# Optimization experiments

Measured on AMD Instinct MI355X. Metric: run time of the kernel, lower is better.

Reference implementation:

```python
import jax, jax.numpy as jnp
import numpy as np

N = 8192          # tokens
CD = 512          # coarse_dim
FD = 512          # fine_dim
CB = 4096         # coarse codebook size
FB = 8192         # fine codebook size
COST = 0.25       # commitment cost
LRELU = 0.1
EPS = 1e-5


def _vq(x, emb):
    # squared-distance cdist: [n, K]
    d = jnp.sum(x * x, axis=1, keepdims=True) + jnp.sum(emb * emb, axis=1) - 2.0 * (x @ emb.T)
    idx = jnp.argmin(d, axis=1)          # temperature=1.0 (updates=0); scaling doesn't change argmin
    q = emb[idx]                          # gather == one-hot @ emb, without materializing one-hot
    e_loss = jnp.mean((jax.lax.stop_gradient(q) - x) ** 2)
    q_loss = jnp.mean((q - jax.lax.stop_gradient(x)) ** 2)
    loss = q_loss + COST * e_loss
    q_st = x + jax.lax.stop_gradient(q - x)   # straight-through
    return q_st, loss


def _mlp(x, w, b, g, be):
    # Linear (torch: x @ W.T + b) -> LayerNorm -> LeakyReLU(0.1)
    h = x @ w.T + b
    m = jnp.mean(h, axis=-1, keepdims=True)
    v = jnp.var(h, axis=-1, keepdims=True)
    h = (h - m) / jnp.sqrt(v + EPS) * g + be
    return jnp.where(h > 0, h, LRELU * h)


def setup_inputs() -> dict:
    key = jax.random.key(0)
    ks = jax.random.split(key, 6)
    xav_c = float(np.sqrt(6.0 / (CB + CD)))
    xav_f = float(np.sqrt(6.0 / (FB + FD)))
    lin_s = float(np.sqrt(1.0 / CD))
    return {
        'z': jax.random.normal(ks[0], (N, CD + FD), dtype=jnp.float32),
        'coarse_emb': jax.random.uniform(ks[1], (CB, CD), jnp.float32, -xav_c, xav_c),
        'fine_emb': jax.random.uniform(ks[2], (FB, FD), jnp.float32, -xav_f, xav_f),
        'w_c2f': jax.random.uniform(ks[3], (FD, CD), jnp.float32, -lin_s, lin_s),
        'b_c2f': jnp.zeros((FD,), jnp.float32),
        'g_c2f': jnp.ones((FD,), jnp.float32),
        'be_c2f': jnp.zeros((FD,), jnp.float32),
        'w_f2c': jax.random.uniform(ks[4], (CD, FD), jnp.float32, -lin_s, lin_s),
        'b_f2c': jnp.zeros((CD,), jnp.float32),
        'g_f2c': jnp.ones((CD,), jnp.float32),
        'be_f2c': jnp.zeros((CD,), jnp.float32),
        'gate_c_raw': jnp.float32(0.5),
        'gate_f_raw': jnp.float32(0.5),
    }


def reference(z, coarse_emb, fine_emb, w_c2f, b_c2f, g_c2f, be_c2f,
              w_f2c, b_f2c, g_f2c, be_f2c, gate_c_raw, gate_f_raw):
    split = z.shape[1] // 2
    z_coarse, z_fine = z[:, :split], z[:, split:]

    z_coarse_q, coarse_loss = _vq(z_coarse, coarse_emb)
    coarse_influence = _mlp(jax.lax.stop_gradient(z_coarse_q), w_c2f, b_c2f, g_c2f, be_c2f)
    gate_c = jax.nn.sigmoid(gate_c_raw)

    residual = z_fine - gate_c * coarse_influence
    z_fine_q, fine_loss = _vq(residual, fine_emb)

    fine_feedback = _mlp(jax.lax.stop_gradient(z_fine_q), w_f2c, b_f2c, g_f2c, be_f2c)
    gate_f = jax.nn.sigmoid(gate_f_raw)

    z_coarse_corrected = z_coarse_q + 0.1 * gate_f * fine_feedback
    z_fine_reconstructed = z_fine_q + gate_c * coarse_influence
    z_hierarchical = jnp.concatenate([z_coarse_corrected, z_fine_reconstructed], axis=1)
    vq_loss = coarse_loss + fine_loss
    return z_hierarchical, vq_loss
```

## Files before the change

kernel.cpp:

```cpp
#include <hip/hip_runtime.h>
#include <hip/hip_bf16.h>
#include <cstdint>
#include <cstddef>

#define KD 512

#define OFF_CN   0u
#define OFF_FN   16384u
#define OFF_ZN   49152u
#define OFF_RN   81920u
#define OFF_LOSS 114688u
#define OFF_AMC  114944u
#define OFF_AMF  180480u
#define OFF_CEH  246016u
#define OFF_CEL  4440320u
#define OFF_FEH  8634624u
#define OFF_FEL  17023232u
#define OFF_ZCH  25411840u
#define OFF_ZCL  33800448u
#define OFF_RH   42189056u
#define OFF_RL   50577664u
#define OFF_W1H  58966272u
#define OFF_W1L  59490560u
#define OFF_W2H  60014848u
#define OFF_W2L  60539136u
#define OFF_H    61063424u
#define OFF_INFL 77840640u


typedef __attribute__((ext_vector_type(8))) short bf16x8;
typedef __attribute__((ext_vector_type(4))) float f32x4;
typedef unsigned long long u64;

__device__ __forceinline__ bf16x8 as_bf16x8(int4 v) {
  union { int4 i; bf16x8 b; } u; u.i = v; return u.b;
}

__device__ __forceinline__ void gl_lds16(const void* g, void* l) {
  __builtin_amdgcn_global_load_lds(
      (const __attribute__((address_space(1))) void*)g,
      (__attribute__((address_space(3))) void*)l, 16, 0, 0);
}

__device__ __forceinline__ float block_sum(float v, float* sred) {
#pragma unroll
  for (int off = 32; off > 0; off >>= 1) v += __shfl_down(v, off, 64);
  if ((threadIdx.x & 63) == 0) sred[threadIdx.x >> 6] = v;
  __syncthreads();
  float r = sred[0] + sred[1] + sred[2] + sred[3];
  __syncthreads();
  return r;
}

__device__ __forceinline__ float sigmoidf_(float x) { return 1.0f / (1.0f + expf(-x)); }

__device__ __forceinline__ void split_bf16(float v, __hip_bfloat16* hi, __hip_bfloat16* lo) {
  __hip_bfloat16 h = __float2bfloat16(v);
  *hi = h;
  *lo = __float2bfloat16(v - __bfloat162float(h));
}

__device__ __forceinline__ unsigned enc_sortable(float f) {
  unsigned u = __float_as_uint(f);
  return (u & 0x80000000u) ? ~u : (u | 0x80000000u);
}
__device__ __forceinline__ float dec_sortable(unsigned ub) {
  unsigned o = (ub & 0x80000000u) ? (ub & 0x7fffffffu) : ~ub;
  return __uint_as_float(o);
}
__device__ __forceinline__ u64 umin64(u64 a, u64 b) { return a < b ? a : b; }
__device__ __forceinline__ u64 umax64(u64 a, u64 b) { return a > b ? a : b; }

__device__ __forceinline__ void merge3(u64& a1, u64& a2, u64& a3, u64 b1, u64 b2, u64 b3) {
  u64 p = umax64(a1, b1);
  u64 q = umin64(a2, b2);
  u64 r = umax64(a2, b2);
  u64 s = umin64(a3, b3);
  u64 m1 = umin64(a1, b1);
  u64 m2 = umin64(p, q);
  u64 m3 = umin64(umin64(umax64(p, q), r), s);
  a1 = m1; a2 = m2; a3 = m3;
}

__global__ __launch_bounds__(256) void prep(
    const float* __restrict__ ce, const float* __restrict__ fe, const float* __restrict__ z,
    const float* __restrict__ w1, const float* __restrict__ w2,
    float* __restrict__ cn, float* __restrict__ fn, float* __restrict__ zn,
    __hip_bfloat16* __restrict__ ceH, __hip_bfloat16* __restrict__ ceL,
    __hip_bfloat16* __restrict__ feH, __hip_bfloat16* __restrict__ feL,
    __hip_bfloat16* __restrict__ zcH,
    __hip_bfloat16* __restrict__ w1H, __hip_bfloat16* __restrict__ w1L,
    __hip_bfloat16* __restrict__ w2H, __hip_bfloat16* __restrict__ w2L,
    float* __restrict__ lossp) {
  __shared__ float sred[4];
  const int b = blockIdx.x, t = threadIdx.x;
  const float* src;
  float* nd = nullptr;
  __hip_bfloat16 *dh = nullptr, *dl = nullptr;
  int fragMode = 0, hiOnly = 0;
  size_t row;
  if (b < 4096) {
    row = b; src = ce + row * KD; nd = cn + row; dh = ceH; dl = ceL; fragMode = 1;
  } else if (b < 12288) {
    row = b - 4096; src = fe + row * KD; nd = fn + row; dh = feH; dl = feL; fragMode = 1;
  } else if (b < 20480) {
    row = b - 12288; src = z + row * 1024; nd = zn + row; dh = zcH; hiOnly = 1;
  } else if (b < 20992) {
    row = b - 20480; src = w1 + row * KD; dh = w1H; dl = w1L;
  } else {
    row = b - 20992; src = w2 + row * KD; dh = w2H; dl = w2L;
  }
  float acc = 0.0f;
  if (fragMode) {
    float v0 = src[t], v1 = src[t + 256];
    acc = v0 * v0 + v1 * v1;
  } else {
#pragma unroll
    for (int j = 0; j < 2; ++j) {
      int c = t + j * 256;
      float v = src[c];
      acc += v * v;
      __hip_bfloat16 h, l;
      split_bf16(v, &h, &l);
      dh[row * KD + c] = h;
      if (!hiOnly) dl[row * KD + c] = l;
    }
  }
  if (nd) {
    float s = block_sum(acc, sred);
    if (t == 0) nd[0] = s;
  } else {
    __syncthreads();
    __syncthreads();
  }
  if (fragMode && t < 64) {
    union { int4 i; __hip_bfloat16 s[8]; } ph, pl;
#pragma unroll
    for (int j = 0; j < 8; ++j) {
      float v = src[8 * t + j];
      split_bf16(v, &ph.s[j], &pl.s[j]);
    }
    const int chunkIdx = (int)(((row >> 4) * 16 + (t >> 2)) * 64 +
                               ((size_t)((t & 3) << 4) | (row & 15)));
    ((int4*)dh)[chunkIdx] = ph.i;
    ((int4*)dl)[chunkIdx] = pl.i;
  }
  if (b == 20480 && t == 0) lossp[0] = 0.0f;
}

__global__ __launch_bounds__(256) void vq8(
    const int4* __restrict__ AfH,
    const __hip_bfloat16* __restrict__ Bh,
    const float* __restrict__ cn,
    u64* __restrict__ bkeys) {
  __shared__ __align__(16) __hip_bfloat16 sBh[3][128 * 32];
  const int t = threadIdx.x;
  const int w = t >> 6, l = t & 63;
  const int rowTile = blockIdx.y << 7;
  const int colTile = blockIdx.x << 7;
  const int NB = gridDim.y;
  const int wr = (w >> 1) << 6;
  const int wc = (w & 1) << 6;

  const int rl = l >> 2;
  const int sbp = (l & 3) ^ ((l >> 3) & 3);
  const size_t gOff0 = (size_t)(colTile + (w << 5) + rl) * KD + (sbp << 3);
  const size_t gOff1 = gOff0 + (size_t)16 * KD;
  const int lOff0 = (w << 5) << 5;
  const int lOff1 = lOff0 + (16 << 5);

  const int fr = l & 15;
  const int q = l >> 4;

  int aB[4];
#pragma unroll
  for (int mt = 0; mt < 4; ++mt)
    aB[mt] = (((rowTile + wr + (mt << 4)) >> 4) << 10) + l;

  f32x4 acc[4][4];
#pragma unroll
  for (int i = 0; i < 4; ++i)
#pragma unroll
    for (int j = 0; j < 4; ++j) acc[i][j] = (f32x4){0.f, 0.f, 0.f, 0.f};

#define STAGE_B(bi, ck) do {                                      \
    gl_lds16(Bh + gOff0 + ((size_t)(ck) << 5), &sBh[bi][lOff0]);  \
    gl_lds16(Bh + gOff1 + ((size_t)(ck) << 5), &sBh[bi][lOff1]);  \
  } while (0)

  int4 aH[4];
  STAGE_B(0, 0);
  STAGE_B(1, 1);
#pragma unroll
  for (int mt = 0; mt < 4; ++mt) aH[mt] = AfH[aB[mt]];
  __builtin_amdgcn_sched_barrier(0);
  asm volatile("s_waitcnt vmcnt(0)" ::: "memory");

#pragma unroll
  for (int i = 0; i < 16; ++i) {
    __builtin_amdgcn_s_barrier();
    __builtin_amdgcn_sched_barrier(0);
    if (i + 2 < 16) STAGE_B((i + 2) % 3, i + 2);
    __builtin_amdgcn_sched_barrier(0);

    bf16x8 afh[4];
#pragma unroll
    for (int mt = 0; mt < 4; ++mt) afh[mt] = as_bf16x8(aH[mt]);
    if (i + 1 < 16) {
#pragma unroll
      for (int mt = 0; mt < 4; ++mt) aH[mt] = AfH[aB[mt] + ((i + 1) << 6)];
    }
    __builtin_amdgcn_sched_barrier(0);

    __builtin_amdgcn_s_setprio(1);
    const int cb = i % 3;
    bf16x8 bfh[4];
#pragma unroll
    for (int nt = 0; nt < 4; ++nt) {
      const int rB = wc + (nt << 4) + fr;
      const int o = (rB << 5) + ((q ^ ((rB >> 1) & 3)) << 3);
      bfh[nt] = *(const bf16x8*)(sBh[cb] + o);
    }
#pragma unroll
    for (int mt = 0; mt < 4; ++mt)
#pragma unroll
      for (int nt = 0; nt < 4; ++nt)
        acc[mt][nt] = __builtin_amdgcn_mfma_f32_16x16x32_bf16(afh[mt], bfh[nt], acc[mt][nt], 0, 0, 0);
    __builtin_amdgcn_s_setprio(0);
  }
#undef STAGE_B

  u64 tk1[4], tk2[4], tk3[4];
#pragma unroll
  for (int nt = 0; nt < 4; ++nt) {
    u64 t1 = ~0ULL, t2 = ~0ULL, t3 = ~0ULL;
#pragma unroll
    for (int mt = 0; mt < 4; ++mt) {
#pragma unroll
      for (int reg = 0; reg < 4; ++reg) {
        const int code = rowTile + wr + (mt << 4) + (q << 2) + reg;
        float d = cn[code] - 2.0f * acc[mt][nt][reg];
        u64 key = ((u64)enc_sortable(d) << 32) | (u64)(unsigned)code;
        if (key < t1) { t3 = t2; t2 = t1; t1 = key; }
        else if (key < t2) { t3 = t2; t2 = key; }
        else if (key < t3) { t3 = key; }
      }
    }
#pragma unroll
    for (int off = 16; off <= 32; off <<= 1) {
      u64 b1 = __shfl_xor(t1, off, 64);
      u64 b2 = __shfl_xor(t2, off, 64);
      u64 b3 = __shfl_xor(t3, off, 64);
      merge3(t1, t2, t3, b1, b2, b3);
    }
    tk1[nt] = t1; tk2[nt] = t2; tk3[nt] = t3;
  }

  __syncthreads();
  u64* sk = (u64*)sBh;
  if (w >= 2 && l < 16) {
#pragma unroll
    for (int nt = 0; nt < 4; ++nt) {
      const int o = ((((w & 1) << 2) + nt) * 16 + fr) * 3;
      sk[o] = tk1[nt]; sk[o + 1] = tk2[nt]; sk[o + 2] = tk3[nt];
    }
  }
  __syncthreads();
  if (w < 2 && l < 16) {
#pragma unroll
    for (int nt = 0; nt < 4; ++nt) {
      const int o = (((w << 2) + nt) * 16 + fr) * 3;
      u64 t1 = tk1[nt], t2 = tk2[nt], t3 = tk3[nt];
      merge3(t1, t2, t3, sk[o], sk[o + 1], sk[o + 2]);
      const int query = colTile + wc + (nt << 4) + fr;
      const size_t bo = ((size_t)query * NB + blockIdx.y) * 3;
      bkeys[bo] = t1; bkeys[bo + 1] = t2; bkeys[bo + 2] = t3;
    }
  }
}

__global__ __launch_bounds__(256) void rescue(
    const u64* __restrict__ bkeys, int NB3,
    const float* __restrict__ Q, int qStride,
    const float* __restrict__ Cb,
    const float* __restrict__ qn, const float* __restrict__ cnorm,
    float dscale, u64* __restrict__ am) {
  const int wv = threadIdx.x >> 6, l = threadIdx.x & 63;
  const int qi = (blockIdx.x << 2) + wv;
  const u64* kq = bkeys + (size_t)qi * NB3;
  u64 kk[3];
#pragma unroll
  for (int j = 0; j < 3; ++j) {
    const int idx = l + (j << 6);
    kk[j] = (idx < NB3) ? kq[idx] : ~0ULL;
  }
  u64 kmin = umin64(kk[0], umin64(kk[1], kk[2]));
#pragma unroll
  for (int off = 32; off > 0; off >>= 1) kmin = umin64(kmin, __shfl_xor(kmin, off, 64));
  const float xnv = qn[qi];
  const float dmin = dec_sortable((unsigned)(kmin >> 32));
  const float thr = dmin + dscale * sqrtf(xnv) + 0.01f;
  const u64 thrKey = ((u64)enc_sortable(thr) << 32) | 0xffffffffULL;

  const float* qrow = Q + (size_t)qi * qStride;
  const float4 qa = *(const float4*)(qrow + (l << 3));
  const float4 qb = *(const float4*)(qrow + (l << 3) + 4);
  float bestD = 3.4e38f;
  int bestC = 0x7fffffff;
#pragma unroll
  for (int j = 0; j < 3; ++j) {
    bool pend = kk[j] <= thrKey;
    u64 mask;
    while ((mask = __ballot(pend)) != 0ULL) {
      const int src = __ffsll((unsigned long long)mask) - 1;
      const u64 key = __shfl(kk[j], src, 64);
      if (l == src) pend = false;
      const int code = (int)(unsigned)(key & 0xffffffffULL);
      const float* crow = Cb + (size_t)code * KD;
      const float4 ca = *(const float4*)(crow + (l << 3));
      const float4 cb = *(const float4*)(crow + (l << 3) + 4);
      float dt = qa.x * ca.x + qa.y * ca.y + qa.z * ca.z + qa.w * ca.w +
                 qb.x * cb.x + qb.y * cb.y + qb.z * cb.z + qb.w * cb.w;
#pragma unroll
      for (int off = 32; off > 0; off >>= 1) dt += __shfl_xor(dt, off, 64);
      const float d = (xnv + cnorm[code]) - 2.0f * dt;
      if (d < bestD || (d == bestD && code < bestC)) { bestD = d; bestC = code; }
    }
  }
  if (l == 0) am[qi] = ((u64)enc_sortable(bestD) << 32) | (unsigned)bestC;
}

__global__ __launch_bounds__(256) void mlp6(
    const int4* __restrict__ AfH, const int4* __restrict__ AfL,
    const u64* __restrict__ gather,
    const __hip_bfloat16* __restrict__ Bh, const __hip_bfloat16* __restrict__ Bl,
    const float* __restrict__ bias, float* __restrict__ C) {
  __shared__ __align__(16) __hip_bfloat16 sAh[128 * 32];
  __shared__ __align__(16) __hip_bfloat16 sAl[128 * 32];
  __shared__ __align__(16) __hip_bfloat16 sBh[128 * 32];
  __shared__ __align__(16) __hip_bfloat16 sBl[128 * 32];
  const int t = threadIdx.x;
  const int w = t >> 6, l = t & 63;
  const int rowTile = blockIdx.y << 7;
  const int colTile = blockIdx.x << 7;
  const int wr = (w >> 1) << 6;
  const int wc = (w & 1) << 6;

  const int srow = t >> 2;
  const int sb = t & 3;
  const int skE = sb << 3;
  const int swz = (sb ^ ((srow >> 1) & 3)) << 3;
  const int wOff0 = (srow << 5) + swz;
  const int wOff1 = ((srow + 64) << 5) + swz;

  unsigned i0 = ((const unsigned*)gather)[2 * (rowTile + srow)];
  unsigned i1 = ((const unsigned*)gather)[2 * (rowTile + 64 + srow)];
  const int a0 = (int)((i0 >> 4) << 10) + (sb << 4) + (int)(i0 & 15);
  const int a1 = (int)((i1 >> 4) << 10) + (sb << 4) + (int)(i1 & 15);
  const size_t br0 = (size_t)(colTile + srow) * KD;
  const size_t br1 = (size_t)(colTile + 64 + srow) * KD;

  const int fr = l & 15;
  const int q = l >> 4;

  f32x4 acc[4][4];
#pragma unroll
  for (int i = 0; i < 4; ++i)
#pragma unroll
    for (int j = 0; j < 4; ++j) acc[i][j] = (f32x4){0.f, 0.f, 0.f, 0.f};

  for (int kk = 0; kk < KD; kk += 32) {
    const int kc64 = (kk >> 5) << 6;
    int4 vAh0 = AfH[a0 + kc64];
    int4 vAh1 = AfH[a1 + kc64];
    int4 vAl0 = AfL[a0 + kc64];
    int4 vAl1 = AfL[a1 + kc64];
    int4 vBh0 = *(const int4*)(Bh + br0 + kk + skE);
    int4 vBh1 = *(const int4*)(Bh + br1 + kk + skE);
    int4 vBl0 = *(const int4*)(Bl + br0 + kk + skE);
    int4 vBl1 = *(const int4*)(Bl + br1 + kk + skE);
    __syncthreads();
    *(int4*)(sAh + wOff0) = vAh0; *(int4*)(sAh + wOff1) = vAh1;
    *(int4*)(sAl + wOff0) = vAl0; *(int4*)(sAl + wOff1) = vAl1;
    *(int4*)(sBh + wOff0) = vBh0; *(int4*)(sBh + wOff1) = vBh1;
    *(int4*)(sBl + wOff0) = vBl0; *(int4*)(sBl + wOff1) = vBl1;
    __syncthreads();

    bf16x8 afh[4], afl[4], bfh[4], bfl[4];
#pragma unroll
    for (int mt = 0; mt < 4; ++mt) {
      const int rA = wr + (mt << 4) + fr;
      const int o = (rA << 5) + ((q ^ ((rA >> 1) & 3)) << 3);
      afh[mt] = *(const bf16x8*)(sAh + o);
      afl[mt] = *(const bf16x8*)(sAl + o);
    }
#pragma unroll
    for (int nt = 0; nt < 4; ++nt) {
      const int rB = wc + (nt << 4) + fr;
      const int o = (rB << 5) + ((q ^ ((rB >> 1) & 3)) << 3);
      bfh[nt] = *(const bf16x8*)(sBh + o);
      bfl[nt] = *(const bf16x8*)(sBl + o);
    }
#pragma unroll
    for (int mt = 0; mt < 4; ++mt)
#pragma unroll
      for (int nt = 0; nt < 4; ++nt) {
        acc[mt][nt] = __builtin_amdgcn_mfma_f32_16x16x32_bf16(afh[mt], bfh[nt], acc[mt][nt], 0, 0, 0);
        acc[mt][nt] = __builtin_amdgcn_mfma_f32_16x16x32_bf16(afh[mt], bfl[nt], acc[mt][nt], 0, 0, 0);
        acc[mt][nt] = __builtin_amdgcn_mfma_f32_16x16x32_bf16(afl[mt], bfh[nt], acc[mt][nt], 0, 0, 0);
      }
  }

  const int quad = l >> 4;
#pragma unroll
  for (int mt = 0; mt < 4; ++mt) {
#pragma unroll
    for (int reg = 0; reg < 4; ++reg) {
      const int row = rowTile + wr + (mt << 4) + (quad << 2) + reg;
#pragma unroll
      for (int nt = 0; nt < 4; ++nt) {
        const int col = colTile + wc + (nt << 4) + fr;
        C[(size_t)row * KD + col] = acc[mt][nt][reg] + bias[col];
      }
    }
  }
}

__global__ __launch_bounds__(256) void ln_residual(
    const float* __restrict__ h, const float* __restrict__ g, const float* __restrict__ be,
    const float* __restrict__ z, const float* __restrict__ gRaw,
    __hip_bfloat16* __restrict__ infl, float* __restrict__ rn,
    __hip_bfloat16* __restrict__ rH, float* __restrict__ resF) {
  __shared__ float sred[4];
  const int row = blockIdx.x, t = threadIdx.x;
  const size_t base = (size_t)row * KD;
  float h0 = h[base + t], h1 = h[base + t + 256];
  float m = block_sum(h0 + h1, sred) * (1.0f / 512.0f);
  float d0 = h0 - m, d1 = h1 - m;
  float var = block_sum(d0 * d0 + d1 * d1, sred) * (1.0f / 512.0f);
  float sq = sqrtf(var + 1e-5f);
  float gc = sigmoidf_(gRaw[0]);
  float v0 = d0 / sq * g[t] + be[t];
  float v1 = d1 / sq * g[t + 256] + be[t + 256];
  v0 = v0 > 0.0f ? v0 : 0.1f * v0;
  v1 = v1 > 0.0f ? v1 : 0.1f * v1;
  infl[base + t] = __float2bfloat16(v0);
  infl[base + t + 256] = __float2bfloat16(v1);
  float zf0 = z[(size_t)row * 1024 + 512 + t];
  float zf1 = z[(size_t)row * 1024 + 512 + t + 256];
  float r0 = zf0 - gc * v0, r1 = zf1 - gc * v1;
  rH[base + t] = __float2bfloat16(r0);
  rH[base + t + 256] = __float2bfloat16(r1);
  resF[base + t] = r0;
  resF[base + t + 256] = r1;
  float rs = block_sum(r0 * r0 + r1 * r1, sred);
  if (t == 0) rn[row] = rs;
}

__global__ __launch_bounds__(256) void finalize(
    const float* __restrict__ h, const float* __restrict__ g, const float* __restrict__ be,
    const __hip_bfloat16* __restrict__ infl,
    const u64* __restrict__ amc, const u64* __restrict__ amf,
    const float* __restrict__ z, const float* __restrict__ ce, const float* __restrict__ fe,
    const float* __restrict__ gcRaw, const float* __restrict__ gfRaw,
    float* __restrict__ out, float* __restrict__ lossp) {
  __shared__ float sred[4];
  const int row = blockIdx.x, t = threadIdx.x;
  const size_t base = (size_t)row * KD;
  float h0 = h[base + t], h1 = h[base + t + 256];
  float m = block_sum(h0 + h1, sred) * (1.0f / 512.0f);
  float d0 = h0 - m, d1 = h1 - m;
  float var = block_sum(d0 * d0 + d1 * d1, sred) * (1.0f / 512.0f);
  float sq = sqrtf(var + 1e-5f);
  float fb0 = d0 / sq * g[t] + be[t];
  float fb1 = d1 / sq * g[t + 256] + be[t + 256];
  fb0 = fb0 > 0.0f ? fb0 : 0.1f * fb0;
  fb1 = fb1 > 0.0f ? fb1 : 0.1f * fb1;
  float gc = sigmoidf_(gcRaw[0]);
  float gf = sigmoidf_(gfRaw[0]);
  unsigned ic = (unsigned)(amc[row] & 0xffffffffULL);
  unsigned ifx = (unsigned)(amf[row] & 0xffffffffULL);
  float loc = 0.0f;
#pragma unroll
  for (int j = 0; j < 2; ++j) {
    int c = t + j * 256;
    float fb = j ? fb1 : fb0;
    float qc = ce[(size_t)ic * KD + c];
    float qf = fe[(size_t)ifx * KD + c];
    float zc = z[(size_t)row * 1024 + c];
    float zf = z[(size_t)row * 1024 + 512 + c];
    float fl = __bfloat162float(infl[base + c]);
    out[(size_t)row * 1024 + c] = qc + 0.1f * gf * fb;
    out[(size_t)row * 1024 + 512 + c] = qf + gc * fl;
    float dc = qc - zc;
    float res = zf - gc * fl;
    float df = qf - res;
    loc += dc * dc + df * df;
  }
  float ls = block_sum(loc, sred);
  if (t == 0) atomicAdd(lossp, ls);
}

__global__ void loss_write(const float* __restrict__ lossp, float* __restrict__ out) {
  out[0] = 1.25f * lossp[0] / (8192.0f * 512.0f);
}

extern "C" void kernel_launch(void* const* d_in, const int* in_sizes, int n_in,
                              void* d_out, int out_size, void* d_ws, size_t ws_size,
                              hipStream_t stream) {
  const float* z      = (const float*)d_in[0];
  const float* ce     = (const float*)d_in[1];
  const float* fe     = (const float*)d_in[2];
  const float* w_c2f  = (const float*)d_in[3];
  const float* b_c2f  = (const float*)d_in[4];
  const float* g_c2f  = (const float*)d_in[5];
  const float* be_c2f = (const float*)d_in[6];
  const float* w_f2c  = (const float*)d_in[7];
  const float* b_f2c  = (const float*)d_in[8];
  const float* g_f2c  = (const float*)d_in[9];
  const float* be_f2c = (const float*)d_in[10];
  const float* gcRaw  = (const float*)d_in[11];
  const float* gfRaw  = (const float*)d_in[12];
  float* out = (float*)d_out;
  char* ws = (char*)d_ws;

  float* cn = (float*)(ws + OFF_CN);
  float* fn = (float*)(ws + OFF_FN);
  float* zn = (float*)(ws + OFF_ZN);
  float* rn = (float*)(ws + OFF_RN);
  float* lossp = (float*)(ws + OFF_LOSS);
  u64* amc = (u64*)(ws + OFF_AMC);
  u64* amf = (u64*)(ws + OFF_AMF);
  __hip_bfloat16* ceH = (__hip_bfloat16*)(ws + OFF_CEH);
  __hip_bfloat16* ceL = (__hip_bfloat16*)(ws + OFF_CEL);
  __hip_bfloat16* feH = (__hip_bfloat16*)(ws + OFF_FEH);
  __hip_bfloat16* feL = (__hip_bfloat16*)(ws + OFF_FEL);
  __hip_bfloat16* zcH = (__hip_bfloat16*)(ws + OFF_ZCH);
  __hip_bfloat16* rH  = (__hip_bfloat16*)(ws + OFF_RH);
  __hip_bfloat16* w1H = (__hip_bfloat16*)(ws + OFF_W1H);
  __hip_bfloat16* w1L = (__hip_bfloat16*)(ws + OFF_W1L);
  __hip_bfloat16* w2H = (__hip_bfloat16*)(ws + OFF_W2H);
  __hip_bfloat16* w2L = (__hip_bfloat16*)(ws + OFF_W2L);
  float* h = (float*)(ws + OFF_H);
  __hip_bfloat16* infl = (__hip_bfloat16*)(ws + OFF_INFL);
  u64* bkeys = (u64*)(ws + OFF_H);
  float* resF = (float*)(ws + OFF_ZCH);

  prep<<<21504, 256, 0, stream>>>(ce, fe, z, w_c2f, w_f2c, cn, fn, zn,
                                  ceH, ceL, feH, feL, zcH,
                                  w1H, w1L, w2H, w2L, lossp);

  vq8<<<dim3(64, 32), 256, 0, stream>>>((const int4*)ceH, zcH, cn, bkeys);

  rescue<<<2048, 256, 0, stream>>>(bkeys, 96, z, 1024, ce, zn, cn, 0.00321f, amc);

  mlp6<<<dim3(4, 64), 256, 0, stream>>>((const int4*)ceH, (const int4*)ceL, amc,
                                        w1H, w1L, b_c2f, h);

  ln_residual<<<8192, 256, 0, stream>>>(h, g_c2f, be_c2f, z, gcRaw, infl, rn, rH, resF);

  vq8<<<dim3(64, 64), 256, 0, stream>>>((const int4*)feH, rH, fn, bkeys);

  rescue<<<2048, 256, 0, stream>>>(bkeys, 192, resF, 512, fe, rn, fn, 0.00233f, amf);

  mlp6<<<dim3(4, 64), 256, 0, stream>>>((const int4*)feH, (const int4*)feL, amf,
                                        w2H, w2L, b_f2c, h);

  finalize<<<8192, 256, 0, stream>>>(h, g_f2c, be_f2c, infl, amc, amf, z, ce, fe,
                                     gcRaw, gfRaw, out, lossp);
  loss_write<<<1, 1, 0, stream>>>(lossp, out + (size_t)8192 * 1024);
}
```

Baseline: 563.3 us.

## Stage codebook A-fragments through LDS and remap blocks per XCD in VQ GEMM

The VQ distance GEMM kernel now loads the codebook (A) fragments into a triple-buffered LDS ring with async global-to-LDS copies, alongside the B tiles, instead of per-wave register prefetch from global memory. Waits are now explicit vmcnt counts so the pipeline keeps two stages in flight. It also remaps block IDs so each XCD handles a contiguous band of codebook row tiles, which is meant to improve L2 reuse of A. This costs extra LDS capacity and LDS read traffic, and relies on hand-counted waitcnts being correct.

```diff
diff --git a/kernel.cpp b/kernel.cpp
--- a/kernel.cpp
+++ b/kernel.cpp
@@ -148,16 +148,24 @@
   if (b == 20480 && t == 0) lossp[0] = 0.0f;
 }
 
-__global__ __launch_bounds__(256) void vq8(
+__global__ __launch_bounds__(256) void vq9(
     const int4* __restrict__ AfH,
     const __hip_bfloat16* __restrict__ Bh,
     const float* __restrict__ cn,
     u64* __restrict__ bkeys) {
-  __shared__ __align__(16) __hip_bfloat16 sBh[3][128 * 32];
+  __shared__ __align__(16) int4 sA[3][512];
+  __shared__ __align__(16) __hip_bfloat16 sB[3][128 * 32];
   const int t = threadIdx.x;
   const int w = t >> 6, l = t & 63;
-  const int rowTile = blockIdx.y << 7;
-  const int colTile = blockIdx.x << 7;
+
+  const int id = (int)blockIdx.x + ((int)gridDim.x) * (int)blockIdx.y;
+  const int xcd = id & 7;
+  const int ix = id >> 3;
+  const int ypp = (int)gridDim.y >> 3;
+  const int bx = ix & 63;
+  const int by = xcd * ypp + (ix >> 6);
+  const int rowTile = by << 7;
+  const int colTile = bx << 7;
   const int NB = gridDim.y;
   const int wr = (w >> 1) << 6;
   const int wc = (w & 1) << 6;
@@ -166,61 +174,55 @@
   const int sbp = (l & 3) ^ ((l >> 3) & 3);
   const size_t gOff0 = (size_t)(colTile + (w << 5) + rl) * KD + (sbp << 3);
   const size_t gOff1 = gOff0 + (size_t)16 * KD;
-  const int lOff0 = (w << 5) << 5;
-  const int lOff1 = lOff0 + (16 << 5);
+  const int lOffB0 = (w << 5) << 5;
+  const int lOffB1 = lOffB0 + (16 << 5);
+
+  const int rtg = rowTile >> 4;
+  const int aS0 = ((rtg + 2 * w) << 10) + l;
+  const int aS1 = ((rtg + 2 * w + 1) << 10) + l;
 
   const int fr = l & 15;
   const int q = l >> 4;
 
-  int aB[4];
-#pragma unroll
-  for (int mt = 0; mt < 4; ++mt)
-    aB[mt] = (((rowTile + wr + (mt << 4)) >> 4) << 10) + l;
-
   f32x4 acc[4][4];
 #pragma unroll
   for (int i = 0; i < 4; ++i)
 #pragma unroll
     for (int j = 0; j < 4; ++j) acc[i][j] = (f32x4){0.f, 0.f, 0.f, 0.f};
 
-#define STAGE_B(bi, ck) do {                                      \
-    gl_lds16(Bh + gOff0 + ((size_t)(ck) << 5), &sBh[bi][lOff0]);  \
-    gl_lds16(Bh + gOff1 + ((size_t)(ck) << 5), &sBh[bi][lOff1]);  \
+#define STAGE(ck) do {                                                   \
+    const int sl_ = (ck) % 3;                                            \
+    gl_lds16(AfH + aS0 + ((ck) << 6), &sA[sl_][(2 * w) << 6]);           \
+    gl_lds16(AfH + aS1 + ((ck) << 6), &sA[sl_][(2 * w + 1) << 6]);       \
+    gl_lds16(Bh + gOff0 + ((size_t)(ck) << 5), &sB[sl_][lOffB0]);        \
+    gl_lds16(Bh + gOff1 + ((size_t)(ck) << 5), &sB[sl_][lOffB1]);        \
   } while (0)
 
-  int4 aH[4];
-  STAGE_B(0, 0);
-  STAGE_B(1, 1);
-#pragma unroll
-  for (int mt = 0; mt < 4; ++mt) aH[mt] = AfH[aB[mt]];
+  STAGE(0);
+  STAGE(1);
   __builtin_amdgcn_sched_barrier(0);
-  asm volatile("s_waitcnt vmcnt(0)" ::: "memory");
 
 #pragma unroll
   for (int i = 0; i < 16; ++i) {
+    if (i < 15) asm volatile("s_waitcnt vmcnt(4) lgkmcnt(0)" ::: "memory");
+    else        asm volatile("s_waitcnt vmcnt(0) lgkmcnt(0)" ::: "memory");
     __builtin_amdgcn_s_barrier();
     __builtin_amdgcn_sched_barrier(0);
-    if (i + 2 < 16) STAGE_B((i + 2) % 3, i + 2);
+    if (i + 2 < 16) STAGE(i + 2);
     __builtin_amdgcn_sched_barrier(0);
 
-    bf16x8 afh[4];
-#pragma unroll
-    for (int mt = 0; mt < 4; ++mt) afh[mt] = as_bf16x8(aH[mt]);
-    if (i + 1 < 16) {
-#pragma unroll
-      for (int mt = 0; mt < 4; ++mt) aH[mt] = AfH[aB[mt] + ((i + 1) << 6)];
-    }
-    __builtin_amdgcn_sched_barrier(0);
-
-    __builtin_amdgcn_s_setprio(1);
     const int cb = i % 3;
-    bf16x8 bfh[4];
+    bf16x8 afh[4], bfh[4];
+#pragma unroll
+    for (int mt = 0; mt < 4; ++mt)
+      afh[mt] = as_bf16x8(sA[cb][(((w >> 1) << 2) + mt) * 64 + l]);
 #pragma unroll
     for (int nt = 0; nt < 4; ++nt) {
       const int rB = wc + (nt << 4) + fr;
       const int o = (rB << 5) + ((q ^ ((rB >> 1) & 3)) << 3);
-      bfh[nt] = *(const bf16x8*)(sBh[cb] + o);
-    }
+      bfh[nt] = *(const bf16x8*)(sB[cb] + o);
+    }
+    __builtin_amdgcn_s_setprio(1);
 #pragma unroll
     for (int mt = 0; mt < 4; ++mt)
 #pragma unroll
@@ -228,7 +230,7 @@
         acc[mt][nt] = __builtin_amdgcn_mfma_f32_16x16x32_bf16(afh[mt], bfh[nt], acc[mt][nt], 0, 0, 0);
     __builtin_amdgcn_s_setprio(0);
   }
-#undef STAGE_B
+#undef STAGE
 
   u64 tk1[4], tk2[4], tk3[4];
 #pragma unroll
@@ -257,7 +259,7 @@
   }
 
   __syncthreads();
-  u64* sk = (u64*)sBh;
+  u64* sk = (u64*)sA;
   if (w >= 2 && l < 16) {
 #pragma unroll
     for (int nt = 0; nt < 4; ++nt) {
@@ -273,7 +275,7 @@
       u64 t1 = tk1[nt], t2 = tk2[nt], t3 = tk3[nt];
       merge3(t1, t2, t3, sk[o], sk[o + 1], sk[o + 2]);
       const int query = colTile + wc + (nt << 4) + fr;
-      const size_t bo = ((size_t)query * NB + blockIdx.y) * 3;
+      const size_t bo = ((size_t)query * NB + by) * 3;
       bkeys[bo] = t1; bkeys[bo + 1] = t2; bkeys[bo + 2] = t3;
     }
   }
@@ -550,7 +552,7 @@
                                   ceH, ceL, feH, feL, zcH,
                                   w1H, w1L, w2H, w2L, lossp);
 
-  vq8<<<dim3(64, 32), 256, 0, stream>>>((const int4*)ceH, zcH, cn, bkeys);
+  vq9<<<dim3(64, 32), 256, 0, stream>>>((const int4*)ceH, zcH, cn, bkeys);
 
   rescue<<<2048, 256, 0, stream>>>(bkeys, 96, z, 1024, ce, zn, cn, 0.00321f, amc);
 
@@ -559,7 +561,7 @@
 
   ln_residual<<<8192, 256, 0, stream>>>(h, g_c2f, be_c2f, z, gcRaw, infl, rn, rH, resF);
 
-  vq8<<<dim3(64, 64), 256, 0, stream>>>((const int4*)feH, rH, fn, bkeys);
+  vq9<<<dim3(64, 64), 256, 0, stream>>>((const int4*)feH, rH, fn, bkeys);
 
   rescue<<<2048, 256, 0, stream>>>(bkeys, 192, resF, 512, fe, rn, fn, 0.00233f, amf);
 
```

After: 589.6 us. +4.7%, slower.
